# Kernel optimization log

Hardware: AMD Instinct MI355X
Metric: run time of the kernel (lower is better)

Reference implementation:

```python
import jax, jax.numpy as jnp
import numpy as np

B, N, D = 4, 8192, 3
BIG = 1e9  # large finite value to invalidate masked points in min-reduction

def setup_inputs() -> dict:
    key = jax.random.key(0)
    k1, k2, k3, k4 = jax.random.split(key, 4)
    pred = jax.random.normal(k1, (B, N, D), jnp.float32) * 0.05
    target = jax.random.normal(k2, (B, N, D), jnp.float32) * 0.05
    points = jax.random.normal(k3, (B, N, D), jnp.float32)
    mask = jax.random.randint(k4, (B, N), 0, 2).astype(jnp.int32)
    return {"pred": pred, "target": target, "mask": mask, "points": points}

def reference(pred, target, mask, points):
    m = mask.astype(pred.dtype)  # [B, N]
    # masked L1 term: per-point mean over coords, masked mean over all points
    l1 = jnp.abs(pred - target).mean(-1)          # [B, N]
    l1 = (l1 * m).sum() / m.sum()
    # Chamfer between clean and predicted denoised points (squared L2, pytorch3d norm=2)
    clean = points + target                        # [B, N, 3]
    predp = points + pred                          # [B, N, 3]
    d2 = (jnp.sum(clean * clean, -1)[:, :, None]
          + jnp.sum(predp * predp, -1)[:, None, :]
          - 2.0 * jnp.einsum('bnd,bmd->bnm', clean, predp))  # [B, N, N]
    d2 = jnp.maximum(d2, 0.0)
    inv = (1.0 - m) * BIG                          # [B, N], penalty for masked-out points
    min_x = jnp.min(d2 + inv[:, None, :], axis=2)  # [B, N] nearest pred point for each clean
    min_y = jnp.min(d2 + inv[:, :, None], axis=1)  # [B, N] nearest clean point for each pred
    count = jnp.maximum(m.sum(-1), 1.0)            # valid points per batch
    cham = (min_x * m).sum(-1) / count + (min_y * m).sum(-1) / count  # [B]
    cd = cham.sum() / B
    return 0.5 * (l1 + cd)
```

## Files before the change

### kernel.cpp

```cpp
#include <hip/hip_runtime.h>
#include <stdint.h>

#define NPTS 8192
#define BATCH 4
#define CHUNK 512
#define NJX (NPTS / CHUNK)

typedef __attribute__((ext_vector_type(8))) short bf16x8;
typedef __attribute__((ext_vector_type(16))) float f32x16;

struct Accum {
  float l1sum;
  float count[BATCH];
  float minsum[8];
  unsigned int ticket;
  float pad[2];
};

__device__ __forceinline__ unsigned short f2bf(float x) {
  union { float f; unsigned u; } v; v.f = x;
  unsigned r = v.u + 0x7FFFu + ((v.u >> 16) & 1u);
  return (unsigned short)(r >> 16);
}
__device__ __forceinline__ float bf2f(unsigned short h) {
  union { float f; unsigned u; } v; v.u = ((unsigned)h) << 16;
  return v.f;
}

using as1_t = __attribute__((address_space(1))) const unsigned int;
using as3_t = __attribute__((address_space(3))) unsigned int;
__device__ __forceinline__ void lds_load16(const void* g, void* l) {
  __builtin_amdgcn_global_load_lds((as1_t*)g, (as3_t*)l, 16, 0, 0);
}

__device__ __forceinline__ void writeA(uint4* P, int T, int n,
                                       float x, float y, float z, float nn) {
  float ax = -2.f * x, ay = -2.f * y, az = -2.f * z;
  unsigned xh = f2bf(ax), xl = f2bf(ax - bf2f(xh));
  unsigned yh = f2bf(ay), yl = f2bf(ay - bf2f(yh));
  unsigned zh = f2bf(az), zl = f2bf(az - bf2f(zh));
  unsigned nh = f2bf(nn);
  float rem = nn - bf2f((unsigned short)nh);
  unsigned nm = f2bf(rem);
  unsigned nl = f2bf(rem - bf2f((unsigned short)nm));
  uint4 h0, h1;
  h0.x = xh | (xh << 16); h0.y = xl | (xl << 16);
  h0.z = yh | (yh << 16); h0.w = yl | (yl << 16);
  h1.x = zh | (zh << 16); h1.y = zl | (zl << 16);
  h1.z = nh | (nm << 16); h1.w = nl;
  P[T * 64 + n] = h0;
  P[T * 64 + 32 + n] = h1;
}
__device__ __forceinline__ void writeB(uint4* P, int T, int n,
                                       float x, float y, float z) {
  unsigned xh = f2bf(x), xl = f2bf(x - bf2f((unsigned short)xh));
  unsigned yh = f2bf(y), yl = f2bf(y - bf2f((unsigned short)yh));
  unsigned zh = f2bf(z), zl = f2bf(z - bf2f((unsigned short)zh));
  const unsigned ONE = 0x3F80u;
  unsigned ux = xh | (xl << 16), uy = yh | (yl << 16), uz = zh | (zl << 16);
  uint4 h0, h1;
  h0.x = ux; h0.y = ux; h0.z = uy; h0.w = uy;
  h1.x = uz; h1.y = uz; h1.z = ONE | (ONE << 16); h1.w = ONE;
  P[T * 64 + n] = h0;
  P[T * 64 + 32 + n] = h1;
}

__global__ __launch_bounds__(256) void prep_kernel(
    const float* __restrict__ pred, const float* __restrict__ target,
    const int* __restrict__ mask, const float* __restrict__ points,
    uint4* __restrict__ Apred, uint4* __restrict__ Aclean,
    uint4* __restrict__ Bclean, uint4* __restrict__ Bpred,
    float* __restrict__ qnClean, float* __restrict__ qnPred,
    float* __restrict__ l1part, Accum* __restrict__ acc) {
  int tid = threadIdx.x;
  int g = blockIdx.x * 256 + tid;
  if (g < 16) ((unsigned int*)acc)[g] = 0u;
  float px = pred[3 * g], py = pred[3 * g + 1], pz = pred[3 * g + 2];
  float tx = target[3 * g], ty = target[3 * g + 1], tz = target[3 * g + 2];
  float ox = points[3 * g], oy = points[3 * g + 1], oz = points[3 * g + 2];
  int m = mask[g];
  float cx = ox + tx, cy = oy + ty, cz = oz + tz;
  float qx = ox + px, qy = oy + py, qz = oz + pz;
  float cn = cx * cx + cy * cy + cz * cz;
  float qn = qx * qx + qy * qy + qz * qz;
  float pen = m ? 0.f : 1e9f;
  qnClean[g] = cn;
  qnPred[g] = qn;
  int T = g >> 5, n = g & 31;
  writeA(Apred, T, n, qx, qy, qz, qn + pen);
  writeA(Aclean, T, n, cx, cy, cz, cn + pen);
  writeB(Bclean, T, n, cx, cy, cz);
  writeB(Bpred, T, n, qx, qy, qz);

  float fm = (float)m;
  float l1c = fm * (fabsf(px - tx) + fabsf(py - ty) + fabsf(pz - tz)) * (1.f / 3.f);
  for (int off = 32; off; off >>= 1) l1c += __shfl_down(l1c, off);
  __shared__ float pl[4];
  if ((tid & 63) == 0) pl[tid >> 6] = l1c;
  __syncthreads();
  if (tid == 0) l1part[blockIdx.x] = pl[0] + pl[1] + pl[2] + pl[3];
}

__global__ __launch_bounds__(256) void chamfer_kernel(
    const uint4* __restrict__ Apred, const uint4* __restrict__ Aclean,
    const uint4* __restrict__ Bclean, const uint4* __restrict__ Bpred,
    float* __restrict__ partial) {
  __shared__ uint4 Asm[1024];
  int z = blockIdx.z, dir = z >> 2, b = z & 3;
  const uint4* __restrict__ Ag = dir ? Aclean : Apred;
  const uint4* __restrict__ Bg = dir ? Bpred : Bclean;
  int jx = blockIdx.x, jbase = jx * CHUNK;
  int qbase = blockIdx.y * CHUNK;
  int tid = threadIdx.x;

  const uint4* Agp = Ag + (size_t)(b * NPTS + jbase) * 2;
#pragma unroll
  for (int it = 0; it < 4; it++) lds_load16(Agp + it * 256 + tid, &Asm[it * 256 + tid]);

  int lane = tid & 63, w = tid >> 6, n = lane & 31;
  const bf16x8* Bb = (const bf16x8*)(Bg + (size_t)(b * NPTS + qbase) * 2);
  bf16x8 bfr[4];
  float acc[4];
#pragma unroll
  for (int q = 0; q < 4; q++) {
    bfr[q] = Bb[(w * 4 + q) * 64 + lane];
    acc[q] = 1e30f;
  }
  __syncthreads();

  const bf16x8* Al = (const bf16x8*)Asm;
  f32x16 zacc = {0.f, 0.f, 0.f, 0.f, 0.f, 0.f, 0.f, 0.f,
                 0.f, 0.f, 0.f, 0.f, 0.f, 0.f, 0.f, 0.f};

#pragma unroll 4
  for (int p = 0; p < 16; p++) {
    bf16x8 af = Al[p * 64 + lane];
#pragma unroll
    for (int q = 0; q < 4; q++) {
      f32x16 d = __builtin_amdgcn_mfma_f32_32x32x16_bf16(af, bfr[q], zacc, 0, 0, 0);
      acc[q] = fminf(fminf(d[0], d[1]), acc[q]);
      acc[q] = fminf(fminf(d[2], d[3]), acc[q]);
      acc[q] = fminf(fminf(d[4], d[5]), acc[q]);
      acc[q] = fminf(fminf(d[6], d[7]), acc[q]);
      acc[q] = fminf(fminf(d[8], d[9]), acc[q]);
      acc[q] = fminf(fminf(d[10], d[11]), acc[q]);
      acc[q] = fminf(fminf(d[12], d[13]), acc[q]);
      acc[q] = fminf(fminf(d[14], d[15]), acc[q]);
    }
  }

  float* __restrict__ Pq = partial + ((size_t)(z * NJX + jx)) * NPTS + qbase;
#pragma unroll
  for (int q = 0; q < 4; q++) {
    float v = fminf(acc[q], __shfl_xor(acc[q], 32));
    if (lane < 32) Pq[(w * 4 + q) * 32 + n] = v;
  }
}

__global__ __launch_bounds__(256) void reduce_kernel(
    const int* __restrict__ mask, const float* __restrict__ partial,
    const float* __restrict__ qnClean, const float* __restrict__ qnPred,
    const float* __restrict__ l1part, Accum* __restrict__ acc,
    float* __restrict__ out) {
  int slice = blockIdx.x >> 3, sub = blockIdx.x & 7;
  int dir = slice >> 2, bb = slice & 3;
  int t = threadIdx.x;
  const float4* __restrict__ qn4 =
      (const float4*)((dir ? qnPred : qnClean) + bb * NPTS + sub * 1024);
  const int4* __restrict__ mk4 = (const int4*)(mask + bb * NPTS + sub * 1024);
  const float* __restrict__ P = partial + (size_t)slice * NJX * NPTS + sub * 1024;

  float4 v = ((const float4*)P)[t];
#pragma unroll
  for (int j = 1; j < NJX; j++) {
    float4 u = *(const float4*)(P + (size_t)j * NPTS + 4 * t);
    v.x = fminf(v.x, u.x); v.y = fminf(v.y, u.y);
    v.z = fminf(v.z, u.z); v.w = fminf(v.w, u.w);
  }
  float4 qv = qn4[t];
  int4 mm = mk4[t];
  float s = mm.x * fmaxf(v.x + qv.x, 0.f) + mm.y * fmaxf(v.y + qv.y, 0.f) +
            mm.z * fmaxf(v.z + qv.z, 0.f) + mm.w * fmaxf(v.w + qv.w, 0.f);
  float c = (float)(mm.x + mm.y + mm.z + mm.w);
  for (int off = 32; off; off >>= 1) {
    s += __shfl_down(s, off);
    c += __shfl_down(c, off);
  }
  __shared__ float rs[4], rc[4];
  int wave = t >> 6;
  if ((t & 63) == 0) { rs[wave] = s; rc[wave] = c; }
  __syncthreads();
  if (t == 0) {
    atomicAdd(&acc->minsum[slice], rs[0] + rs[1] + rs[2] + rs[3]);
    if (dir == 0) atomicAdd(&acc->count[bb], rc[0] + rc[1] + rc[2] + rc[3]);
  }

  __threadfence();
  __shared__ unsigned int tk;
  if (t == 0) tk = atomicAdd(&acc->ticket, 1u);
  __syncthreads();
  if (tk != 63u) return;

  float l1 = (t < 128) ? l1part[t] : 0.f;
  for (int off = 32; off; off >>= 1) l1 += __shfl_down(l1, off);
  if ((t & 63) == 0) rs[t >> 6] = l1;
  __syncthreads();
  if (t == 0) {
    float l1s = rs[0] + rs[1];
    float msum = 0.f, cham = 0.f;
#pragma unroll
    for (int b = 0; b < BATCH; b++) {
      float cnt = atomicAdd(&acc->count[b], 0.f);
      float m0 = atomicAdd(&acc->minsum[b], 0.f);
      float m1 = atomicAdd(&acc->minsum[4 + b], 0.f);
      msum += cnt;
      cham += (m0 + m1) / fmaxf(cnt, 1.f);
    }
    out[0] = 0.5f * (l1s / msum + cham * (1.f / BATCH));
  }
}

extern "C" void kernel_launch(void* const* d_in, const int* in_sizes, int n_in,
                              void* d_out, int out_size, void* d_ws, size_t ws_size,
                              hipStream_t stream) {
  const float* pred   = (const float*)d_in[0];
  const float* target = (const float*)d_in[1];
  const int*   mask   = (const int*)d_in[2];
  const float* points = (const float*)d_in[3];
  float* out = (float*)d_out;

  const int NP = BATCH * NPTS;
  uint4* Apred  = (uint4*)d_ws;
  uint4* Aclean = Apred + NP * 2;
  uint4* Bclean = Aclean + NP * 2;
  uint4* Bpred  = Bclean + NP * 2;
  float* qnClean = (float*)(Bpred + NP * 2);
  float* qnPred  = qnClean + NP;
  float* partial = qnPred + NP;
  float* l1part  = partial + 8 * NJX * NPTS;
  Accum* acc     = (Accum*)(l1part + 128);

  prep_kernel<<<NP / 256, 256, 0, stream>>>(
      pred, target, mask, points, Apred, Aclean, Bclean, Bpred,
      qnClean, qnPred, l1part, acc);

  dim3 grid(NJX, NPTS / CHUNK, 2 * BATCH);
  chamfer_kernel<<<grid, 256, 0, stream>>>(
      Apred, Aclean, Bclean, Bpred, partial);

  reduce_kernel<<<64, 256, 0, stream>>>(
      mask, partial, qnClean, qnPred, l1part, acc, out);
}
```

Measured before the change: 99.07 us.

## Fuse prep stage into chamfer and reduce kernels, dropping one launch

Removes the separate prep kernel. Each chamfer block now computes its own bf16 hi/lo split A and B fragments straight from the raw inputs into LDS and registers. The reduce kernel recomputes the point norms and the masked L1 term itself. This saves one kernel launch and the global round trip of the packed fragments, at the cost of redundant conversion work in every chamfer block (each chunk is rebuilt by 16 blocks) and strided scalar 3-float loads. Accumulator zeroing moves to block (0,0,0) of the chamfer kernel, which relies on kernel ordering against the reduce kernel's atomics.

```diff
diff --git a/kernel.cpp b/kernel.cpp
--- a/kernel.cpp
+++ b/kernel.cpp
@@ -14,7 +14,7 @@
   float count[BATCH];
   float minsum[8];
   unsigned int ticket;
-  float pad[2];
+  unsigned int pad[2];
 };
 
 __device__ __forceinline__ unsigned short f2bf(float x) {
@@ -27,14 +27,8 @@
   return v.f;
 }
 
-using as1_t = __attribute__((address_space(1))) const unsigned int;
-using as3_t = __attribute__((address_space(3))) unsigned int;
-__device__ __forceinline__ void lds_load16(const void* g, void* l) {
-  __builtin_amdgcn_global_load_lds((as1_t*)g, (as3_t*)l, 16, 0, 0);
-}
-
-__device__ __forceinline__ void writeA(uint4* P, int T, int n,
-                                       float x, float y, float z, float nn) {
+__device__ __forceinline__ void writeA_lds(uint4* P, int T, int n,
+                                           float x, float y, float z, float nn) {
   float ax = -2.f * x, ay = -2.f * y, az = -2.f * z;
   unsigned xh = f2bf(ax), xl = f2bf(ax - bf2f(xh));
   unsigned yh = f2bf(ay), yl = f2bf(ay - bf2f(yh));
@@ -51,79 +45,53 @@
   P[T * 64 + n] = h0;
   P[T * 64 + 32 + n] = h1;
 }
-__device__ __forceinline__ void writeB(uint4* P, int T, int n,
-                                       float x, float y, float z) {
-  unsigned xh = f2bf(x), xl = f2bf(x - bf2f((unsigned short)xh));
-  unsigned yh = f2bf(y), yl = f2bf(y - bf2f((unsigned short)yh));
-  unsigned zh = f2bf(z), zl = f2bf(z - bf2f((unsigned short)zh));
-  const unsigned ONE = 0x3F80u;
-  unsigned ux = xh | (xl << 16), uy = yh | (yl << 16), uz = zh | (zl << 16);
-  uint4 h0, h1;
-  h0.x = ux; h0.y = ux; h0.z = uy; h0.w = uy;
-  h1.x = uz; h1.y = uz; h1.z = ONE | (ONE << 16); h1.w = ONE;
-  P[T * 64 + n] = h0;
-  P[T * 64 + 32 + n] = h1;
-}
-
-__global__ __launch_bounds__(256) void prep_kernel(
+
+__global__ __launch_bounds__(256) void chamfer_kernel(
     const float* __restrict__ pred, const float* __restrict__ target,
     const int* __restrict__ mask, const float* __restrict__ points,
-    uint4* __restrict__ Apred, uint4* __restrict__ Aclean,
-    uint4* __restrict__ Bclean, uint4* __restrict__ Bpred,
-    float* __restrict__ qnClean, float* __restrict__ qnPred,
-    float* __restrict__ l1part, Accum* __restrict__ acc) {
-  int tid = threadIdx.x;
-  int g = blockIdx.x * 256 + tid;
-  if (g < 16) ((unsigned int*)acc)[g] = 0u;
-  float px = pred[3 * g], py = pred[3 * g + 1], pz = pred[3 * g + 2];
-  float tx = target[3 * g], ty = target[3 * g + 1], tz = target[3 * g + 2];
-  float ox = points[3 * g], oy = points[3 * g + 1], oz = points[3 * g + 2];
-  int m = mask[g];
-  float cx = ox + tx, cy = oy + ty, cz = oz + tz;
-  float qx = ox + px, qy = oy + py, qz = oz + pz;
-  float cn = cx * cx + cy * cy + cz * cz;
-  float qn = qx * qx + qy * qy + qz * qz;
-  float pen = m ? 0.f : 1e9f;
-  qnClean[g] = cn;
-  qnPred[g] = qn;
-  int T = g >> 5, n = g & 31;
-  writeA(Apred, T, n, qx, qy, qz, qn + pen);
-  writeA(Aclean, T, n, cx, cy, cz, cn + pen);
-  writeB(Bclean, T, n, cx, cy, cz);
-  writeB(Bpred, T, n, qx, qy, qz);
-
-  float fm = (float)m;
-  float l1c = fm * (fabsf(px - tx) + fabsf(py - ty) + fabsf(pz - tz)) * (1.f / 3.f);
-  for (int off = 32; off; off >>= 1) l1c += __shfl_down(l1c, off);
-  __shared__ float pl[4];
-  if ((tid & 63) == 0) pl[tid >> 6] = l1c;
-  __syncthreads();
-  if (tid == 0) l1part[blockIdx.x] = pl[0] + pl[1] + pl[2] + pl[3];
-}
-
-__global__ __launch_bounds__(256) void chamfer_kernel(
-    const uint4* __restrict__ Apred, const uint4* __restrict__ Aclean,
-    const uint4* __restrict__ Bclean, const uint4* __restrict__ Bpred,
-    float* __restrict__ partial) {
+    float* __restrict__ partial, Accum* __restrict__ accg) {
   __shared__ uint4 Asm[1024];
   int z = blockIdx.z, dir = z >> 2, b = z & 3;
-  const uint4* __restrict__ Ag = dir ? Aclean : Apred;
-  const uint4* __restrict__ Bg = dir ? Bpred : Bclean;
-  int jx = blockIdx.x, jbase = jx * CHUNK;
+  const float* __restrict__ dr = dir ? target : pred;
+  const float* __restrict__ dq = dir ? pred : target;
+  int jbase = blockIdx.x * CHUNK;
   int qbase = blockIdx.y * CHUNK;
   int tid = threadIdx.x;
 
-  const uint4* Agp = Ag + (size_t)(b * NPTS + jbase) * 2;
-#pragma unroll
-  for (int it = 0; it < 4; it++) lds_load16(Agp + it * 256 + tid, &Asm[it * 256 + tid]);
-
-  int lane = tid & 63, w = tid >> 6, n = lane & 31;
-  const bf16x8* Bb = (const bf16x8*)(Bg + (size_t)(b * NPTS + qbase) * 2);
-  bf16x8 bfr[4];
+  if (blockIdx.x == 0 && blockIdx.y == 0 && z == 0 && tid < 16)
+    atomicExch((unsigned int*)accg + tid, 0u);
+
+  for (int i = tid; i < CHUNK; i += 256) {
+    int g = b * NPTS + jbase + i;
+    float rx = points[3 * g] + dr[3 * g];
+    float ry = points[3 * g + 1] + dr[3 * g + 1];
+    float rz = points[3 * g + 2] + dr[3 * g + 2];
+    float rn = rx * rx + ry * ry + rz * rz + (mask[g] ? 0.f : 1e9f);
+    writeA_lds(Asm, i >> 5, i & 31, rx, ry, rz, rn);
+  }
+
+  int lane = tid & 63, w = tid >> 6, n = lane & 31, h = lane >> 5;
+  const unsigned ONE = 0x3F80u;
+  union Frag { bf16x8 v; unsigned u[4]; };
+  Frag bfr[4];
   float acc[4];
 #pragma unroll
   for (int q = 0; q < 4; q++) {
-    bfr[q] = Bb[(w * 4 + q) * 64 + lane];
+    int g = b * NPTS + qbase + (w * 4 + q) * 32 + n;
+    float qx = points[3 * g] + dq[3 * g];
+    float qy = points[3 * g + 1] + dq[3 * g + 1];
+    float qz = points[3 * g + 2] + dq[3 * g + 2];
+    if (h == 0) {
+      unsigned xh = f2bf(qx), xl = f2bf(qx - bf2f((unsigned short)xh));
+      unsigned yh = f2bf(qy), yl = f2bf(qy - bf2f((unsigned short)yh));
+      unsigned ux = xh | (xl << 16), uy = yh | (yl << 16);
+      bfr[q].u[0] = ux; bfr[q].u[1] = ux; bfr[q].u[2] = uy; bfr[q].u[3] = uy;
+    } else {
+      unsigned zh = f2bf(qz), zl = f2bf(qz - bf2f((unsigned short)zh));
+      unsigned uz = zh | (zl << 16);
+      bfr[q].u[0] = uz; bfr[q].u[1] = uz;
+      bfr[q].u[2] = ONE | (ONE << 16); bfr[q].u[3] = ONE;
+    }
     acc[q] = 1e30f;
   }
   __syncthreads();
@@ -137,7 +105,7 @@
     bf16x8 af = Al[p * 64 + lane];
 #pragma unroll
     for (int q = 0; q < 4; q++) {
-      f32x16 d = __builtin_amdgcn_mfma_f32_32x32x16_bf16(af, bfr[q], zacc, 0, 0, 0);
+      f32x16 d = __builtin_amdgcn_mfma_f32_32x32x16_bf16(af, bfr[q].v, zacc, 0, 0, 0);
       acc[q] = fminf(fminf(d[0], d[1]), acc[q]);
       acc[q] = fminf(fminf(d[2], d[3]), acc[q]);
       acc[q] = fminf(fminf(d[4], d[5]), acc[q]);
@@ -149,7 +117,7 @@
     }
   }
 
-  float* __restrict__ Pq = partial + ((size_t)(z * NJX + jx)) * NPTS + qbase;
+  float* __restrict__ Pq = partial + ((size_t)(z * NJX + blockIdx.x)) * NPTS + qbase;
 #pragma unroll
   for (int q = 0; q < 4; q++) {
     float v = fminf(acc[q], __shfl_xor(acc[q], 32));
@@ -158,16 +126,15 @@
 }
 
 __global__ __launch_bounds__(256) void reduce_kernel(
-    const int* __restrict__ mask, const float* __restrict__ partial,
-    const float* __restrict__ qnClean, const float* __restrict__ qnPred,
-    const float* __restrict__ l1part, Accum* __restrict__ acc,
+    const float* __restrict__ pred, const float* __restrict__ target,
+    const int* __restrict__ mask, const float* __restrict__ points,
+    const float* __restrict__ partial, Accum* __restrict__ acc,
     float* __restrict__ out) {
   int slice = blockIdx.x >> 3, sub = blockIdx.x & 7;
   int dir = slice >> 2, bb = slice & 3;
+  const float* __restrict__ dq = dir ? pred : target;
   int t = threadIdx.x;
-  const float4* __restrict__ qn4 =
-      (const float4*)((dir ? qnPred : qnClean) + bb * NPTS + sub * 1024);
-  const int4* __restrict__ mk4 = (const int4*)(mask + bb * NPTS + sub * 1024);
+  int base = bb * NPTS + sub * 1024;
   const float* __restrict__ P = partial + (size_t)slice * NJX * NPTS + sub * 1024;
 
   float4 v = ((const float4*)P)[t];
@@ -177,22 +144,38 @@
     v.x = fminf(v.x, u.x); v.y = fminf(v.y, u.y);
     v.z = fminf(v.z, u.z); v.w = fminf(v.w, u.w);
   }
-  float4 qv = qn4[t];
-  int4 mm = mk4[t];
-  float s = mm.x * fmaxf(v.x + qv.x, 0.f) + mm.y * fmaxf(v.y + qv.y, 0.f) +
-            mm.z * fmaxf(v.z + qv.z, 0.f) + mm.w * fmaxf(v.w + qv.w, 0.f);
-  float c = (float)(mm.x + mm.y + mm.z + mm.w);
+  float vv[4] = {v.x, v.y, v.z, v.w};
+  float s = 0.f, c = 0.f, l1 = 0.f;
+#pragma unroll
+  for (int k = 0; k < 4; k++) {
+    int g = base + 4 * t + k;
+    float qx = points[3 * g] + dq[3 * g];
+    float qy = points[3 * g + 1] + dq[3 * g + 1];
+    float qz = points[3 * g + 2] + dq[3 * g + 2];
+    float qn = qx * qx + qy * qy + qz * qz;
+    float m = (float)mask[g];
+    s += m * fmaxf(vv[k] + qn, 0.f);
+    c += m;
+    if (dir == 0)
+      l1 += m * (fabsf(pred[3 * g] - target[3 * g]) +
+                 fabsf(pred[3 * g + 1] - target[3 * g + 1]) +
+                 fabsf(pred[3 * g + 2] - target[3 * g + 2])) * (1.f / 3.f);
+  }
   for (int off = 32; off; off >>= 1) {
     s += __shfl_down(s, off);
     c += __shfl_down(c, off);
-  }
-  __shared__ float rs[4], rc[4];
+    l1 += __shfl_down(l1, off);
+  }
+  __shared__ float rs[4], rc[4], rl[4];
   int wave = t >> 6;
-  if ((t & 63) == 0) { rs[wave] = s; rc[wave] = c; }
+  if ((t & 63) == 0) { rs[wave] = s; rc[wave] = c; rl[wave] = l1; }
   __syncthreads();
   if (t == 0) {
     atomicAdd(&acc->minsum[slice], rs[0] + rs[1] + rs[2] + rs[3]);
-    if (dir == 0) atomicAdd(&acc->count[bb], rc[0] + rc[1] + rc[2] + rc[3]);
+    if (dir == 0) {
+      atomicAdd(&acc->count[bb], rc[0] + rc[1] + rc[2] + rc[3]);
+      atomicAdd(&acc->l1sum, rl[0] + rl[1] + rl[2] + rl[3]);
+    }
   }
 
   __threadfence();
@@ -200,13 +183,8 @@
   if (t == 0) tk = atomicAdd(&acc->ticket, 1u);
   __syncthreads();
   if (tk != 63u) return;
-
-  float l1 = (t < 128) ? l1part[t] : 0.f;
-  for (int off = 32; off; off >>= 1) l1 += __shfl_down(l1, off);
-  if ((t & 63) == 0) rs[t >> 6] = l1;
-  __syncthreads();
   if (t == 0) {
-    float l1s = rs[0] + rs[1];
+    float l1s = atomicAdd(&acc->l1sum, 0.f);
     float msum = 0.f, cham = 0.f;
 #pragma unroll
     for (int b = 0; b < BATCH; b++) {
@@ -229,25 +207,11 @@
   const float* points = (const float*)d_in[3];
   float* out = (float*)d_out;
 
-  const int NP = BATCH * NPTS;
-  uint4* Apred  = (uint4*)d_ws;
-  uint4* Aclean = Apred + NP * 2;
-  uint4* Bclean = Aclean + NP * 2;
-  uint4* Bpred  = Bclean + NP * 2;
-  float* qnClean = (float*)(Bpred + NP * 2);
-  float* qnPred  = qnClean + NP;
-  float* partial = qnPred + NP;
-  float* l1part  = partial + 8 * NJX * NPTS;
-  Accum* acc     = (Accum*)(l1part + 128);
-
-  prep_kernel<<<NP / 256, 256, 0, stream>>>(
-      pred, target, mask, points, Apred, Aclean, Bclean, Bpred,
-      qnClean, qnPred, l1part, acc);
+  float* partial = (float*)d_ws;
+  Accum* acc = (Accum*)(partial + 8 * NJX * NPTS);
 
   dim3 grid(NJX, NPTS / CHUNK, 2 * BATCH);
-  chamfer_kernel<<<grid, 256, 0, stream>>>(
-      Apred, Aclean, Bclean, Bpred, partial);
-
-  reduce_kernel<<<64, 256, 0, stream>>>(
-      mask, partial, qnClean, qnPred, l1part, acc, out);
-}
+  chamfer_kernel<<<grid, 256, 0, stream>>>(pred, target, mask, points, partial, acc);
+
+  reduce_kernel<<<64, 256, 0, stream>>>(pred, target, mask, points, partial, acc, out);
+}
```

Result: faster. 95.65 us (-3.5%).
